# Optimization experiments

Hardware: AMD Instinct MI355X
Metric: run time of the kernel (lower is better)

## Reference

```python
import jax, jax.numpy as jnp
import numpy as np

B, S, D, P, H, DFF = 32, 512, 768, 256, 12, 3072
DH = D // H
EPS_LN = 1e-5
EPS_TRIP = 1e-6
MARGIN = 1.0


def setup_inputs() -> dict:
    key = jax.random.key(0)
    ks = jax.random.split(key, 16)
    sent_emb = jax.random.normal(ks[0], (B, S, D), jnp.float32)
    pair_sidx = jax.random.randint(ks[1], (P,), 0, B, jnp.int32)

    def mk_span(k):
        k1, k2 = jax.random.split(k)
        start = jax.random.randint(k1, (P,), 1, S - 9, jnp.int32)
        length = jax.random.randint(k2, (P,), 1, 9, jnp.int32)
        return jnp.stack([start, start + length], axis=1)  # [P,2] half-open

    s_span = mk_span(ks[2])
    p_span = mk_span(ks[3])
    n_span = mk_span(ks[4])
    sc = 0.02

    def w(k, shape):
        return jax.random.normal(k, shape, jnp.float32) * sc

    return dict(
        sent_emb=sent_emb, pair_sidx=pair_sidx,
        s_span=s_span, p_span=p_span, n_span=n_span,
        Wq=w(ks[5], (D, D)), bq=jnp.zeros((D,), jnp.float32),
        Wk=w(ks[6], (D, D)), bk=jnp.zeros((D,), jnp.float32),
        Wv=w(ks[7], (D, D)), bv=jnp.zeros((D,), jnp.float32),
        Wo=w(ks[8], (D, D)), bo=jnp.zeros((D,), jnp.float32),
        ln1_g=jnp.ones((D,), jnp.float32), ln1_b=jnp.zeros((D,), jnp.float32),
        ln2_g=jnp.ones((D,), jnp.float32), ln2_b=jnp.zeros((D,), jnp.float32),
        W1=w(ks[9], (D, DFF)), b1=jnp.zeros((DFF,), jnp.float32),
        W2=w(ks[10], (DFF, D)), b2=jnp.zeros((D,), jnp.float32),
    )


def _ln(x, g, b):
    m = jnp.mean(x, axis=-1, keepdims=True)
    v = jnp.mean((x - m) ** 2, axis=-1, keepdims=True)
    return (x - m) * jax.lax.rsqrt(v + EPS_LN) * g + b


def reference(sent_emb, pair_sidx, s_span, p_span, n_span,
              Wq, bq, Wk, bk, Wv, bv, Wo, bo,
              ln1_g, ln1_b, ln2_g, ln2_b, W1, b1, W2, b2):
    g = sent_emb[pair_sidx]  # [P,S,D] per-pair gathered sentence
    pos = jnp.arange(S)

    def pool(span):  # ragged mean-pool over [start,end)
        mask = ((pos[None, :] >= span[:, :1]) & (pos[None, :] < span[:, 1:2])).astype(sent_emb.dtype)
        cnt = jnp.sum(mask, axis=-1, keepdims=True)
        return jnp.einsum('ps,psd->pd', mask, g) / cnt

    s_emb = pool(s_span)
    p_emb = pool(p_span)
    n_emb = pool(n_span)
    cls_emb = sent_emb[pair_sidx, 0]           # [P,D]
    mem = jnp.stack([cls_emb, s_emb], axis=1)  # [P,2,D] (cls, source phrase)

    def attend(q):  # 1-query cross-attention over 2 memory slots, per pair
        qh = (q @ Wq + bq).reshape(P, H, DH)
        kh = (mem @ Wk + bk).reshape(P, 2, H, DH)
        vh = (mem @ Wv + bv).reshape(P, 2, H, DH)
        scores = jnp.einsum('phd,pkhd->phk', qh, kh) / np.sqrt(DH).astype(np.float32)
        a = jax.nn.softmax(scores, axis=-1)
        o = jnp.einsum('phk,pkhd->phd', a, vh).reshape(P, D)
        return o @ Wo + bo

    def block(x):  # residual attn + LN + position-wise FFN + LN (dropout=eval/identity)
        h = _ln(x + attend(x), ln1_g, ln1_b)
        f = jnp.maximum(h @ W1 + b1, 0.0) @ W2 + b2
        return _ln(h + f, ln2_g, ln2_b)

    atten_p = block(p_emb)
    atten_n = block(n_emb)
    dp = jnp.linalg.norm(s_emb - atten_p + EPS_TRIP, axis=-1)
    dn = jnp.linalg.norm(s_emb - atten_n + EPS_TRIP, axis=-1)
    return jnp.mean(jnp.maximum(dp - dn + MARGIN, 0.0))
```

## Files before the change

### kernel.cpp

```cpp
#include <hip/hip_runtime.h>
#include <hip/hip_bf16.h>

#define Dsz 768
#define Psz 256
#define Hsz 12
#define DHsz 64
#define DFFsz 3072
#define Msz 512
#define EPS_LN 1e-5f
#define EPS_TRIP 1e-6f

typedef unsigned short u16;
typedef __attribute__((ext_vector_type(8))) short bf16x8;
typedef __attribute__((ext_vector_type(4))) float f32x4;

__device__ __forceinline__ u16 f2bf(float f) {
    __hip_bfloat16 h = __float2bfloat16(f);
    u16 u; __builtin_memcpy(&u, &h, 2); return u;
}

__global__ __launch_bounds__(256) void pool_kernel(
    const float* __restrict__ sent, const int* __restrict__ sidx,
    const int* __restrict__ s_span, const int* __restrict__ p_span,
    const int* __restrict__ n_span,
    float* __restrict__ mem, float* __restrict__ qin,
    u16* __restrict__ memb, u16* __restrict__ qinb)
{
    int p = blockIdx.x;
    int b = sidx[p];
    const float* base = sent + (size_t)b * 512 * Dsz;
    int ss = s_span[2*p], se = s_span[2*p+1];
    int ps = p_span[2*p], pe = p_span[2*p+1];
    int ns = n_span[2*p], ne = n_span[2*p+1];
    float is  = 1.0f / (float)(se - ss);
    float ip  = 1.0f / (float)(pe - ps);
    float in_ = 1.0f / (float)(ne - ns);
    for (int d = threadIdx.x; d < Dsz; d += 256) {
        float cls = base[d];
        float as = 0.f, ap = 0.f, an = 0.f;
        for (int s = ss; s < se; ++s) as += base[(size_t)s*Dsz + d];
        for (int s = ps; s < pe; ++s) ap += base[(size_t)s*Dsz + d];
        for (int s = ns; s < ne; ++s) an += base[(size_t)s*Dsz + d];
        as *= is; ap *= ip; an *= in_;
        mem[(size_t)(2*p+0)*Dsz + d] = cls;
        mem[(size_t)(2*p+1)*Dsz + d] = as;
        qin[(size_t)(0*Psz + p)*Dsz + d] = ap;
        qin[(size_t)(1*Psz + p)*Dsz + d] = an;
        memb[(size_t)(2*p+0)*Dsz + d] = f2bf(cls);
        memb[(size_t)(2*p+1)*Dsz + d] = f2bf(as);
        qinb[(size_t)(0*Psz + p)*Dsz + d] = f2bf(ap);
        qinb[(size_t)(1*Psz + p)*Dsz + d] = f2bf(an);
    }
}

struct CvtArgs {
    const float* src[6];
    u16* dst[6];
    int K[6], N[6];
    int t0[7];
};

__global__ __launch_bounds__(256) void cvt_kernel(CvtArgs ca)
{
    __shared__ float tile[64][65];
    int bid = blockIdx.x;
    int w = 0;
    while (bid >= ca.t0[w+1]) ++w;
    int local = bid - ca.t0[w];
    int K = ca.K[w], N = ca.N[w];
    int ntN = N >> 6;
    int tk = local / ntN, tn = local - tk * ntN;
    int k0 = tk << 6, n0 = tn << 6;
    const float* src = ca.src[w];
    u16* dst = ca.dst[w];
    int t = threadIdx.x;
    int r = t >> 2, q = t & 3;
    #pragma unroll
    for (int j = 0; j < 4; ++j) {
        int c4 = q + j*4;
        float4 v = *(const float4*)(src + (size_t)(k0 + r)*N + n0 + c4*4);
        tile[r][c4*4+0] = v.x; tile[r][c4*4+1] = v.y;
        tile[r][c4*4+2] = v.z; tile[r][c4*4+3] = v.w;
    }
    __syncthreads();
    #pragma unroll
    for (int j = 0; j < 4; ++j) {
        int kc4 = q + j*4;
        ushort4 o;
        o.x = f2bf(tile[kc4*4+0][r]);
        o.y = f2bf(tile[kc4*4+1][r]);
        o.z = f2bf(tile[kc4*4+2][r]);
        o.w = f2bf(tile[kc4*4+3][r]);
        *(ushort4*)(dst + (size_t)(n0 + r)*K + k0 + kc4*4) = o;
    }
}

__device__ __forceinline__ void mfma_gemm_core(
    const u16* __restrict__ A, int lda,
    const u16* __restrict__ WT, int ldw,
    const float* __restrict__ bias,
    float* __restrict__ Cf, u16* __restrict__ Cb, int ldc,
    int Kloop, int relu, int bx, int by)
{
    int tid = threadIdx.x;
    int lane = tid & 63, wave = tid >> 6;
    int wr = wave >> 1, wc = wave & 1;
    int row0 = by*64 + wr*32, col0 = bx*64 + wc*32;
    int r = lane & 15, kg = lane >> 4;
    const u16* Ap0 = A  + (size_t)(row0 + r)      * lda + kg*8;
    const u16* Ap1 = A  + (size_t)(row0 + 16 + r) * lda + kg*8;
    const u16* Bp0 = WT + (size_t)(col0 + r)      * ldw + kg*8;
    const u16* Bp1 = WT + (size_t)(col0 + 16 + r) * ldw + kg*8;
    f32x4 acc00 = {0.f,0.f,0.f,0.f}, acc01 = {0.f,0.f,0.f,0.f};
    f32x4 acc10 = {0.f,0.f,0.f,0.f}, acc11 = {0.f,0.f,0.f,0.f};
    for (int k = 0; k < Kloop; k += 64) {
        bf16x8 a0 = *(const bf16x8*)(Ap0 + k);
        bf16x8 a1 = *(const bf16x8*)(Ap1 + k);
        bf16x8 b0 = *(const bf16x8*)(Bp0 + k);
        bf16x8 b1 = *(const bf16x8*)(Bp1 + k);
        bf16x8 a2 = *(const bf16x8*)(Ap0 + k + 32);
        bf16x8 a3 = *(const bf16x8*)(Ap1 + k + 32);
        bf16x8 b2 = *(const bf16x8*)(Bp0 + k + 32);
        bf16x8 b3 = *(const bf16x8*)(Bp1 + k + 32);
        acc00 = __builtin_amdgcn_mfma_f32_16x16x32_bf16(a0, b0, acc00, 0, 0, 0);
        acc01 = __builtin_amdgcn_mfma_f32_16x16x32_bf16(a0, b1, acc01, 0, 0, 0);
        acc10 = __builtin_amdgcn_mfma_f32_16x16x32_bf16(a1, b0, acc10, 0, 0, 0);
        acc11 = __builtin_amdgcn_mfma_f32_16x16x32_bf16(a1, b1, acc11, 0, 0, 0);
        acc00 = __builtin_amdgcn_mfma_f32_16x16x32_bf16(a2, b2, acc00, 0, 0, 0);
        acc01 = __builtin_amdgcn_mfma_f32_16x16x32_bf16(a2, b3, acc01, 0, 0, 0);
        acc10 = __builtin_amdgcn_mfma_f32_16x16x32_bf16(a3, b2, acc10, 0, 0, 0);
        acc11 = __builtin_amdgcn_mfma_f32_16x16x32_bf16(a3, b3, acc11, 0, 0, 0);
    }
    float b0s = bias ? bias[col0 + r]      : 0.f;
    float b1s = bias ? bias[col0 + 16 + r] : 0.f;
    #pragma unroll
    for (int e = 0; e < 4; ++e) {
        int rr0 = row0 + kg*4 + e;
        int rr1 = rr0 + 16;
        float v00 = acc00[e] + b0s, v01 = acc01[e] + b1s;
        float v10 = acc10[e] + b0s, v11 = acc11[e] + b1s;
        if (relu) {
            v00 = fmaxf(v00, 0.f); v01 = fmaxf(v01, 0.f);
            v10 = fmaxf(v10, 0.f); v11 = fmaxf(v11, 0.f);
        }
        if (Cf) {
            Cf[(size_t)rr0*ldc + col0 + r]      = v00;
            Cf[(size_t)rr0*ldc + col0 + 16 + r] = v01;
            Cf[(size_t)rr1*ldc + col0 + r]      = v10;
            Cf[(size_t)rr1*ldc + col0 + 16 + r] = v11;
        }
        if (Cb) {
            Cb[(size_t)rr0*ldc + col0 + r]      = f2bf(v00);
            Cb[(size_t)rr0*ldc + col0 + 16 + r] = f2bf(v01);
            Cb[(size_t)rr1*ldc + col0 + r]      = f2bf(v10);
            Cb[(size_t)rr1*ldc + col0 + 16 + r] = f2bf(v11);
        }
    }
}

struct Proj3Args {
    const u16* A[3];
    const u16* WT[3];
    const float* bias[3];
    float* C[3];
};
__global__ __launch_bounds__(256) void proj3_mfma(Proj3Args pa)
{
    int j = blockIdx.z;
    mfma_gemm_core(pa.A[j], Dsz, pa.WT[j], Dsz, pa.bias[j],
                   pa.C[j], nullptr, Dsz, Dsz, 0, blockIdx.x, blockIdx.y);
}

__global__ __launch_bounds__(256) void gemm_mfma(
    const u16* __restrict__ A, int lda, const u16* __restrict__ WT, int ldw,
    const float* __restrict__ bias, float* __restrict__ Cf, u16* __restrict__ Cb,
    int ldc, int Kloop, int relu)
{
    mfma_gemm_core(A, lda, WT, ldw, bias, Cf, Cb, ldc, Kloop, relu,
                   blockIdx.x, blockIdx.y);
}

__global__ __launch_bounds__(256) void gemm_mfma_splitk(
    const u16* __restrict__ A, int lda, const u16* __restrict__ WT, int ldw,
    const float* __restrict__ bias, float* __restrict__ Cpart,
    int ldc, int Ks, size_t pstride)
{
    int s = blockIdx.z;
    mfma_gemm_core(A + (size_t)s * Ks, lda, WT + (size_t)s * Ks, ldw,
                   (s == 0) ? bias : nullptr,
                   Cpart + (size_t)s * pstride, nullptr, ldc, Ks, 0,
                   blockIdx.x, blockIdx.y);
}

__global__ __launch_bounds__(64) void attn_kernel(
    const float* __restrict__ qh, const float* __restrict__ kh,
    const float* __restrict__ vh, u16* __restrict__ ob)
{
    int rblk = blockIdx.x;
    int p = rblk & (Psz - 1);
    int lane = threadIdx.x;
    const float* q  = qh + (size_t)rblk * Dsz;
    const float* k0 = kh + (size_t)(2*p) * Dsz;
    const float* k1 = k0 + Dsz;
    const float* v0 = vh + (size_t)(2*p) * Dsz;
    const float* v1 = v0 + Dsz;
    u16* o = ob + (size_t)rblk * Dsz;
    #pragma unroll
    for (int h = 0; h < Hsz; ++h) {
        int idx = h * DHsz + lane;
        float qv = q[idx];
        float s0 = qv * k0[idx];
        float s1 = qv * k1[idx];
        #pragma unroll
        for (int off = 32; off; off >>= 1) {
            s0 += __shfl_xor(s0, off);
            s1 += __shfl_xor(s1, off);
        }
        s0 *= 0.125f;
        s1 *= 0.125f;
        float m = fmaxf(s0, s1);
        float e0 = expf(s0 - m), e1 = expf(s1 - m);
        float inv = 1.f / (e0 + e1);
        o[idx] = f2bf((e0 * inv) * v0[idx] + (e1 * inv) * v1[idx]);
    }
}

__global__ __launch_bounds__(256) void ln_kernel(
    const float* __restrict__ x, const float* __restrict__ y,
    int nparts, size_t pstride,
    const float* __restrict__ g, const float* __restrict__ b,
    float* __restrict__ out, u16* __restrict__ out16)
{
    __shared__ float sb[4];
    int rr = blockIdx.x;
    int t = threadIdx.x;
    float v[3];
    float s = 0.f;
    #pragma unroll
    for (int i = 0; i < 3; ++i) {
        int d = t + i * 256;
        float acc = x[(size_t)rr*Dsz + d];
        for (int q = 0; q < nparts; ++q)
            acc += y[(size_t)q*pstride + (size_t)rr*Dsz + d];
        v[i] = acc;
        s += acc;
    }
    #pragma unroll
    for (int off = 32; off; off >>= 1) s += __shfl_xor(s, off);
    if ((t & 63) == 0) sb[t >> 6] = s;
    __syncthreads();
    float mean = (sb[0] + sb[1] + sb[2] + sb[3]) * (1.0f / Dsz);
    __syncthreads();
    float sv = 0.f;
    #pragma unroll
    for (int i = 0; i < 3; ++i) { float d0 = v[i] - mean; sv += d0 * d0; }
    #pragma unroll
    for (int off = 32; off; off >>= 1) sv += __shfl_xor(sv, off);
    if ((t & 63) == 0) sb[t >> 6] = sv;
    __syncthreads();
    float var = (sb[0] + sb[1] + sb[2] + sb[3]) * (1.0f / Dsz);
    float rstd = 1.0f / sqrtf(var + EPS_LN);
    #pragma unroll
    for (int i = 0; i < 3; ++i) {
        int d = t + i * 256;
        float o = (v[i] - mean) * rstd * g[d] + b[d];
        out[(size_t)rr*Dsz + d] = o;
        if (out16) out16[(size_t)rr*Dsz + d] = f2bf(o);
    }
}

__global__ __launch_bounds__(256) void loss_kernel(
    const float* __restrict__ mem, const float* __restrict__ outb,
    float* __restrict__ d_out)
{
    __shared__ float sb0[4], sb1[4];
    int p = blockIdx.x;
    int t = threadIdx.x;
    const float* se = mem  + (size_t)(2*p+1) * Dsz;
    const float* ap = outb + (size_t)p * Dsz;
    const float* an = outb + (size_t)(Psz + p) * Dsz;
    float dp = 0.f, dn = 0.f;
    #pragma unroll
    for (int i = 0; i < 3; ++i) {
        int d = t + i * 256;
        float a = se[d] - ap[d] + EPS_TRIP; dp += a * a;
        float c = se[d] - an[d] + EPS_TRIP; dn += c * c;
    }
    #pragma unroll
    for (int off = 32; off; off >>= 1) {
        dp += __shfl_xor(dp, off);
        dn += __shfl_xor(dn, off);
    }
    if ((t & 63) == 0) { sb0[t >> 6] = dp; sb1[t >> 6] = dn; }
    __syncthreads();
    if (t == 0) {
        float dps = sqrtf(sb0[0] + sb0[1] + sb0[2] + sb0[3]);
        float dns = sqrtf(sb1[0] + sb1[1] + sb1[2] + sb1[3]);
        float loss = fmaxf(dps - dns + 1.0f, 0.f);
        atomicAdd(d_out, loss * (1.0f / Psz));
    }
}

extern "C" void kernel_launch(void* const* d_in, const int* in_sizes, int n_in,
                              void* d_out, int out_size, void* d_ws, size_t ws_size,
                              hipStream_t stream) {
    const float* sent  = (const float*)d_in[0];
    const int*   sidx  = (const int*)d_in[1];
    const int*   sspan = (const int*)d_in[2];
    const int*   pspan = (const int*)d_in[3];
    const int*   nspan = (const int*)d_in[4];
    const float* Wq = (const float*)d_in[5];
    const float* bq = (const float*)d_in[6];
    const float* Wk = (const float*)d_in[7];
    const float* bk = (const float*)d_in[8];
    const float* Wv = (const float*)d_in[9];
    const float* bv = (const float*)d_in[10];
    const float* Wo = (const float*)d_in[11];
    const float* bo = (const float*)d_in[12];
    const float* ln1g = (const float*)d_in[13];
    const float* ln1b = (const float*)d_in[14];
    const float* ln2g = (const float*)d_in[15];
    const float* ln2b = (const float*)d_in[16];
    const float* W1 = (const float*)d_in[17];
    const float* b1 = (const float*)d_in[18];
    const float* W2 = (const float*)d_in[19];
    const float* b2 = (const float*)d_in[20];
    float* out = (float*)d_out;

    const size_t F = (size_t)Msz * Dsz;
    float* ws   = (float*)d_ws;
    float* mem  = ws + 0*F;
    float* qin  = ws + 1*F;
    float* outbf= ws + 1*F;
    float* hbuf = ws + 2*F;
    float* partb= ws + 3*F;
    float* qh   = ws + 3*F;
    float* kh   = ws + 4*F;
    float* vh   = ws + 5*F;
    u16* memb   = (u16*)(ws + 7*F);
    u16* qinb   = (u16*)(ws + 7*F) + F;
    u16* obufb  = (u16*)(ws + 8*F);
    u16* hbufb  = (u16*)(ws + 8*F) + F;
    u16* f1b    = (u16*)(ws + 9*F);
    u16* WqT    = (u16*)(ws + 11*F);
    u16* WkT    = WqT + (size_t)Dsz*Dsz;
    u16* WvT    = WkT + (size_t)Dsz*Dsz;
    u16* WoT    = WvT + (size_t)Dsz*Dsz;
    u16* W1T    = WoT + (size_t)Dsz*Dsz;
    u16* W2T    = W1T + (size_t)Dsz*DFFsz;

    hipMemsetAsync(d_out, 0, sizeof(float), stream);

    pool_kernel<<<Psz, 256, 0, stream>>>(sent, sidx, sspan, pspan, nspan,
                                         mem, qin, memb, qinb);

    CvtArgs ca;
    ca.src[0]=Wq; ca.src[1]=Wk; ca.src[2]=Wv; ca.src[3]=Wo; ca.src[4]=W1; ca.src[5]=W2;
    ca.dst[0]=WqT; ca.dst[1]=WkT; ca.dst[2]=WvT; ca.dst[3]=WoT; ca.dst[4]=W1T; ca.dst[5]=W2T;
    ca.K[0]=Dsz; ca.K[1]=Dsz; ca.K[2]=Dsz; ca.K[3]=Dsz; ca.K[4]=Dsz;  ca.K[5]=DFFsz;
    ca.N[0]=Dsz; ca.N[1]=Dsz; ca.N[2]=Dsz; ca.N[3]=Dsz; ca.N[4]=DFFsz; ca.N[5]=Dsz;
    int acc_t = 0;
    for (int i = 0; i < 6; ++i) {
        ca.t0[i] = acc_t;
        acc_t += (ca.K[i] >> 6) * (ca.N[i] >> 6);
    }
    ca.t0[6] = acc_t;
    cvt_kernel<<<acc_t, 256, 0, stream>>>(ca);

    Proj3Args pa;
    pa.A[0]=memb; pa.WT[0]=WkT; pa.bias[0]=bk; pa.C[0]=kh;
    pa.A[1]=memb; pa.WT[1]=WvT; pa.bias[1]=bv; pa.C[1]=vh;
    pa.A[2]=qinb; pa.WT[2]=WqT; pa.bias[2]=bq; pa.C[2]=qh;
    proj3_mfma<<<dim3(Dsz/64, Msz/64, 3), 256, 0, stream>>>(pa);

    attn_kernel<<<Msz, 64, 0, stream>>>(qh, kh, vh, obufb);

    gemm_mfma_splitk<<<dim3(Dsz/64, Msz/64, 4), 256, 0, stream>>>(
        obufb, Dsz, WoT, Dsz, bo, partb, Dsz, Dsz/4, F);

    ln_kernel<<<Msz, 256, 0, stream>>>(qin, partb, 4, F, ln1g, ln1b, hbuf, hbufb);

    gemm_mfma<<<dim3(DFFsz/64, Msz/64), 256, 0, stream>>>(
        hbufb, Dsz, W1T, Dsz, b1, nullptr, f1b, DFFsz, Dsz, 1);

    gemm_mfma_splitk<<<dim3(Dsz/64, Msz/64, 4), 256, 0, stream>>>(
        f1b, DFFsz, W2T, DFFsz, b2, partb, Dsz, DFFsz/4, F);

    ln_kernel<<<Msz, 256, 0, stream>>>(hbuf, partb, 4, F, ln2g, ln2b, outbf, nullptr);

    loss_kernel<<<Psz, 256, 0, stream>>>(mem, outbf, out);
}
```

Measured before the change: 265.8 us.

## Fuse whole pipeline into one persistent kernel with atomic grid barriers

Replaces the ten separate launches (pool, weight convert, QKV projection, attention, Wo split-K, LN1, FFN1, FFN2 split-K, LN2, loss) with a single persistent kernel of 256 blocks. The stages are separated by atomic-counter grid barriers. It also fuses the second LayerNorm with the per-row triplet distance and replaces the atomicAdd loss with a final single-block reduction. Split-K goes from 4 to 2 partitions. The aim is to remove launch overhead and intermediate round trips, at the cost of barrier spin time and less parallelism within each stage: 256 blocks cover 384 FFN1 tiles and only 192 split-K tiles, so some stages run partly idle. Correctness depends on all 256 blocks being co-resident.

```diff
diff --git a/kernel.cpp b/kernel.cpp
--- a/kernel.cpp
+++ b/kernel.cpp
@@ -9,6 +9,7 @@
 #define Msz 512
 #define EPS_LN 1e-5f
 #define EPS_TRIP 1e-6f
+#define NBLK 256
 
 typedef unsigned short u16;
 typedef __attribute__((ext_vector_type(8))) short bf16x8;
@@ -19,83 +20,20 @@
     u16 u; __builtin_memcpy(&u, &h, 2); return u;
 }
 
-__global__ __launch_bounds__(256) void pool_kernel(
-    const float* __restrict__ sent, const int* __restrict__ sidx,
-    const int* __restrict__ s_span, const int* __restrict__ p_span,
-    const int* __restrict__ n_span,
-    float* __restrict__ mem, float* __restrict__ qin,
-    u16* __restrict__ memb, u16* __restrict__ qinb)
-{
-    int p = blockIdx.x;
-    int b = sidx[p];
-    const float* base = sent + (size_t)b * 512 * Dsz;
-    int ss = s_span[2*p], se = s_span[2*p+1];
-    int ps = p_span[2*p], pe = p_span[2*p+1];
-    int ns = n_span[2*p], ne = n_span[2*p+1];
-    float is  = 1.0f / (float)(se - ss);
-    float ip  = 1.0f / (float)(pe - ps);
-    float in_ = 1.0f / (float)(ne - ns);
-    for (int d = threadIdx.x; d < Dsz; d += 256) {
-        float cls = base[d];
-        float as = 0.f, ap = 0.f, an = 0.f;
-        for (int s = ss; s < se; ++s) as += base[(size_t)s*Dsz + d];
-        for (int s = ps; s < pe; ++s) ap += base[(size_t)s*Dsz + d];
-        for (int s = ns; s < ne; ++s) an += base[(size_t)s*Dsz + d];
-        as *= is; ap *= ip; an *= in_;
-        mem[(size_t)(2*p+0)*Dsz + d] = cls;
-        mem[(size_t)(2*p+1)*Dsz + d] = as;
-        qin[(size_t)(0*Psz + p)*Dsz + d] = ap;
-        qin[(size_t)(1*Psz + p)*Dsz + d] = an;
-        memb[(size_t)(2*p+0)*Dsz + d] = f2bf(cls);
-        memb[(size_t)(2*p+1)*Dsz + d] = f2bf(as);
-        qinb[(size_t)(0*Psz + p)*Dsz + d] = f2bf(ap);
-        qinb[(size_t)(1*Psz + p)*Dsz + d] = f2bf(an);
-    }
-}
-
-struct CvtArgs {
-    const float* src[6];
-    u16* dst[6];
-    int K[6], N[6];
-    int t0[7];
-};
-
-__global__ __launch_bounds__(256) void cvt_kernel(CvtArgs ca)
-{
-    __shared__ float tile[64][65];
-    int bid = blockIdx.x;
-    int w = 0;
-    while (bid >= ca.t0[w+1]) ++w;
-    int local = bid - ca.t0[w];
-    int K = ca.K[w], N = ca.N[w];
-    int ntN = N >> 6;
-    int tk = local / ntN, tn = local - tk * ntN;
-    int k0 = tk << 6, n0 = tn << 6;
-    const float* src = ca.src[w];
-    u16* dst = ca.dst[w];
-    int t = threadIdx.x;
-    int r = t >> 2, q = t & 3;
-    #pragma unroll
-    for (int j = 0; j < 4; ++j) {
-        int c4 = q + j*4;
-        float4 v = *(const float4*)(src + (size_t)(k0 + r)*N + n0 + c4*4);
-        tile[r][c4*4+0] = v.x; tile[r][c4*4+1] = v.y;
-        tile[r][c4*4+2] = v.z; tile[r][c4*4+3] = v.w;
-    }
+__device__ __forceinline__ void gridbar(unsigned* c) {
     __syncthreads();
-    #pragma unroll
-    for (int j = 0; j < 4; ++j) {
-        int kc4 = q + j*4;
-        ushort4 o;
-        o.x = f2bf(tile[kc4*4+0][r]);
-        o.y = f2bf(tile[kc4*4+1][r]);
-        o.z = f2bf(tile[kc4*4+2][r]);
-        o.w = f2bf(tile[kc4*4+3][r]);
-        *(ushort4*)(dst + (size_t)(n0 + r)*K + k0 + kc4*4) = o;
-    }
-}
-
-__device__ __forceinline__ void mfma_gemm_core(
+    if (threadIdx.x == 0) {
+        __threadfence();
+        __hip_atomic_fetch_add(c, 1u, __ATOMIC_RELEASE, __HIP_MEMORY_SCOPE_AGENT);
+        while (__hip_atomic_load(c, __ATOMIC_ACQUIRE, __HIP_MEMORY_SCOPE_AGENT) < NBLK) {
+            __builtin_amdgcn_s_sleep(1);
+        }
+        __threadfence();
+    }
+    __syncthreads();
+}
+
+__device__ void mfma_tile(
     const u16* __restrict__ A, int lda,
     const u16* __restrict__ WT, int ldw,
     const float* __restrict__ bias,
@@ -158,235 +96,284 @@
     }
 }
 
-struct Proj3Args {
-    const u16* A[3];
-    const u16* WT[3];
-    const float* bias[3];
-    float* C[3];
-};
-__global__ __launch_bounds__(256) void proj3_mfma(Proj3Args pa)
-{
-    int j = blockIdx.z;
-    mfma_gemm_core(pa.A[j], Dsz, pa.WT[j], Dsz, pa.bias[j],
-                   pa.C[j], nullptr, Dsz, Dsz, 0, blockIdx.x, blockIdx.y);
-}
-
-__global__ __launch_bounds__(256) void gemm_mfma(
-    const u16* __restrict__ A, int lda, const u16* __restrict__ WT, int ldw,
-    const float* __restrict__ bias, float* __restrict__ Cf, u16* __restrict__ Cb,
-    int ldc, int Kloop, int relu)
-{
-    mfma_gemm_core(A, lda, WT, ldw, bias, Cf, Cb, ldc, Kloop, relu,
-                   blockIdx.x, blockIdx.y);
-}
-
-__global__ __launch_bounds__(256) void gemm_mfma_splitk(
-    const u16* __restrict__ A, int lda, const u16* __restrict__ WT, int ldw,
-    const float* __restrict__ bias, float* __restrict__ Cpart,
-    int ldc, int Ks, size_t pstride)
-{
-    int s = blockIdx.z;
-    mfma_gemm_core(A + (size_t)s * Ks, lda, WT + (size_t)s * Ks, ldw,
-                   (s == 0) ? bias : nullptr,
-                   Cpart + (size_t)s * pstride, nullptr, ldc, Ks, 0,
-                   blockIdx.x, blockIdx.y);
-}
-
-__global__ __launch_bounds__(64) void attn_kernel(
-    const float* __restrict__ qh, const float* __restrict__ kh,
-    const float* __restrict__ vh, u16* __restrict__ ob)
-{
-    int rblk = blockIdx.x;
-    int p = rblk & (Psz - 1);
-    int lane = threadIdx.x;
-    const float* q  = qh + (size_t)rblk * Dsz;
-    const float* k0 = kh + (size_t)(2*p) * Dsz;
-    const float* k1 = k0 + Dsz;
-    const float* v0 = vh + (size_t)(2*p) * Dsz;
-    const float* v1 = v0 + Dsz;
-    u16* o = ob + (size_t)rblk * Dsz;
-    #pragma unroll
-    for (int h = 0; h < Hsz; ++h) {
-        int idx = h * DHsz + lane;
-        float qv = q[idx];
-        float s0 = qv * k0[idx];
-        float s1 = qv * k1[idx];
-        #pragma unroll
-        for (int off = 32; off; off >>= 1) {
-            s0 += __shfl_xor(s0, off);
-            s1 += __shfl_xor(s1, off);
-        }
-        s0 *= 0.125f;
-        s1 *= 0.125f;
-        float m = fmaxf(s0, s1);
-        float e0 = expf(s0 - m), e1 = expf(s1 - m);
-        float inv = 1.f / (e0 + e1);
-        o[idx] = f2bf((e0 * inv) * v0[idx] + (e1 * inv) * v1[idx]);
-    }
-}
-
-__global__ __launch_bounds__(256) void ln_kernel(
-    const float* __restrict__ x, const float* __restrict__ y,
-    int nparts, size_t pstride,
-    const float* __restrict__ g, const float* __restrict__ b,
-    float* __restrict__ out, u16* __restrict__ out16)
-{
-    __shared__ float sb[4];
-    int rr = blockIdx.x;
-    int t = threadIdx.x;
-    float v[3];
-    float s = 0.f;
-    #pragma unroll
-    for (int i = 0; i < 3; ++i) {
-        int d = t + i * 256;
-        float acc = x[(size_t)rr*Dsz + d];
-        for (int q = 0; q < nparts; ++q)
-            acc += y[(size_t)q*pstride + (size_t)rr*Dsz + d];
-        v[i] = acc;
-        s += acc;
-    }
+__device__ __forceinline__ float blk_sum(float s, float* sb) {
     #pragma unroll
     for (int off = 32; off; off >>= 1) s += __shfl_xor(s, off);
-    if ((t & 63) == 0) sb[t >> 6] = s;
+    if ((threadIdx.x & 63) == 0) sb[threadIdx.x >> 6] = s;
     __syncthreads();
-    float mean = (sb[0] + sb[1] + sb[2] + sb[3]) * (1.0f / Dsz);
+    float tot = sb[0] + sb[1] + sb[2] + sb[3];
     __syncthreads();
-    float sv = 0.f;
-    #pragma unroll
-    for (int i = 0; i < 3; ++i) { float d0 = v[i] - mean; sv += d0 * d0; }
-    #pragma unroll
-    for (int off = 32; off; off >>= 1) sv += __shfl_xor(sv, off);
-    if ((t & 63) == 0) sb[t >> 6] = sv;
-    __syncthreads();
-    float var = (sb[0] + sb[1] + sb[2] + sb[3]) * (1.0f / Dsz);
-    float rstd = 1.0f / sqrtf(var + EPS_LN);
-    #pragma unroll
-    for (int i = 0; i < 3; ++i) {
-        int d = t + i * 256;
-        float o = (v[i] - mean) * rstd * g[d] + b[d];
-        out[(size_t)rr*Dsz + d] = o;
-        if (out16) out16[(size_t)rr*Dsz + d] = f2bf(o);
-    }
-}
-
-__global__ __launch_bounds__(256) void loss_kernel(
-    const float* __restrict__ mem, const float* __restrict__ outb,
-    float* __restrict__ d_out)
+    return tot;
+}
+
+struct FusedArgs {
+    const float* sent; const int* sidx; const int* sspan; const int* pspan; const int* nspan;
+    const float* Wq; const float* bq; const float* Wk; const float* bk;
+    const float* Wv; const float* bv; const float* Wo; const float* bo;
+    const float* ln1g; const float* ln1b; const float* ln2g; const float* ln2b;
+    const float* W1; const float* b1; const float* W2; const float* b2;
+    const float* csrc[6]; u16* cdst[6]; int cK[6], cN[6], ct0[7];
+    float *mem, *qin, *hbuf, *p0, *p1, *qh, *kh, *vh, *rowsq;
+    u16 *memb, *qinb, *obufb, *hbufb, *f1b, *WqT, *WkT, *WvT, *WoT, *W1T, *W2T;
+    unsigned* bar;
+    float* out;
+};
+
+__global__ __launch_bounds__(256, 2) void fused_kernel(FusedArgs a)
 {
-    __shared__ float sb0[4], sb1[4];
-    int p = blockIdx.x;
-    int t = threadIdx.x;
-    const float* se = mem  + (size_t)(2*p+1) * Dsz;
-    const float* ap = outb + (size_t)p * Dsz;
-    const float* an = outb + (size_t)(Psz + p) * Dsz;
-    float dp = 0.f, dn = 0.f;
-    #pragma unroll
-    for (int i = 0; i < 3; ++i) {
-        int d = t + i * 256;
-        float a = se[d] - ap[d] + EPS_TRIP; dp += a * a;
-        float c = se[d] - an[d] + EPS_TRIP; dn += c * c;
-    }
-    #pragma unroll
-    for (int off = 32; off; off >>= 1) {
-        dp += __shfl_xor(dp, off);
-        dn += __shfl_xor(dn, off);
-    }
-    if ((t & 63) == 0) { sb0[t >> 6] = dp; sb1[t >> 6] = dn; }
-    __syncthreads();
-    if (t == 0) {
-        float dps = sqrtf(sb0[0] + sb0[1] + sb0[2] + sb0[3]);
-        float dns = sqrtf(sb1[0] + sb1[1] + sb1[2] + sb1[3]);
-        float loss = fmaxf(dps - dns + 1.0f, 0.f);
-        atomicAdd(d_out, loss * (1.0f / Psz));
+    __shared__ float tile[64][65];
+    __shared__ float sb[4];
+    int b   = blockIdx.x;
+    int tid = threadIdx.x;
+    int wave = tid >> 6, lane = tid & 63;
+
+    {
+        int p = b;
+        int bb = a.sidx[p];
+        const float* base = a.sent + (size_t)bb * 512 * Dsz;
+        int ss = a.sspan[2*p], se = a.sspan[2*p+1];
+        int ps = a.pspan[2*p], pe = a.pspan[2*p+1];
+        int ns = a.nspan[2*p], ne = a.nspan[2*p+1];
+        float is  = 1.0f / (float)(se - ss);
+        float ip  = 1.0f / (float)(pe - ps);
+        float in_ = 1.0f / (float)(ne - ns);
+        for (int d = tid; d < Dsz; d += 256) {
+            float cls = base[d];
+            float as = 0.f, ap = 0.f, an = 0.f;
+            for (int s = ss; s < se; ++s) as += base[(size_t)s*Dsz + d];
+            for (int s = ps; s < pe; ++s) ap += base[(size_t)s*Dsz + d];
+            for (int s = ns; s < ne; ++s) an += base[(size_t)s*Dsz + d];
+            as *= is; ap *= ip; an *= in_;
+            a.mem[(size_t)(2*p+0)*Dsz + d] = cls;
+            a.mem[(size_t)(2*p+1)*Dsz + d] = as;
+            a.qin[(size_t)(0*Psz + p)*Dsz + d] = ap;
+            a.qin[(size_t)(1*Psz + p)*Dsz + d] = an;
+            a.memb[(size_t)(2*p+0)*Dsz + d] = f2bf(cls);
+            a.memb[(size_t)(2*p+1)*Dsz + d] = f2bf(as);
+            a.qinb[(size_t)(0*Psz + p)*Dsz + d] = f2bf(ap);
+            a.qinb[(size_t)(1*Psz + p)*Dsz + d] = f2bf(an);
+        }
+    }
+    for (int t = b; t < 1728; t += NBLK) {
+        __syncthreads();
+        int w = 0;
+        while (t >= a.ct0[w+1]) ++w;
+        int local = t - a.ct0[w];
+        int K = a.cK[w], N = a.cN[w];
+        int ntN = N >> 6;
+        int tk = local / ntN, tn = local - tk * ntN;
+        int k0 = tk << 6, n0 = tn << 6;
+        const float* src = a.csrc[w];
+        u16* dst = a.cdst[w];
+        int rr = tid >> 2, q = tid & 3;
+        #pragma unroll
+        for (int j = 0; j < 4; ++j) {
+            int c4 = q + j*4;
+            float4 v = *(const float4*)(src + (size_t)(k0 + rr)*N + n0 + c4*4);
+            tile[rr][c4*4+0] = v.x; tile[rr][c4*4+1] = v.y;
+            tile[rr][c4*4+2] = v.z; tile[rr][c4*4+3] = v.w;
+        }
+        __syncthreads();
+        #pragma unroll
+        for (int j = 0; j < 4; ++j) {
+            int kc4 = q + j*4;
+            ushort4 o;
+            o.x = f2bf(tile[kc4*4+0][rr]);
+            o.y = f2bf(tile[kc4*4+1][rr]);
+            o.z = f2bf(tile[kc4*4+2][rr]);
+            o.w = f2bf(tile[kc4*4+3][rr]);
+            *(ushort4*)(dst + (size_t)(n0 + rr)*K + k0 + kc4*4) = o;
+        }
+    }
+    gridbar(a.bar + 0);
+
+    for (int t = b; t < 288; t += NBLK) {
+        int j = t / 96, u = t % 96;
+        int bx = u % 12, by = u / 12;
+        const u16* A  = (j == 2) ? a.qinb : a.memb;
+        const u16* WT = (j == 0) ? a.WkT : (j == 1) ? a.WvT : a.WqT;
+        const float* bias = (j == 0) ? a.bk : (j == 1) ? a.bv : a.bq;
+        float* C = (j == 0) ? a.kh : (j == 1) ? a.vh : a.qh;
+        mfma_tile(A, Dsz, WT, Dsz, bias, C, nullptr, Dsz, Dsz, 0, bx, by);
+    }
+    gridbar(a.bar + 1);
+
+    {
+        int rrow = 2*b + (wave >> 1);
+        int p = rrow & (Psz - 1);
+        int hseg = (wave & 1) * 6;
+        const float* q  = a.qh + (size_t)rrow * Dsz;
+        const float* k0 = a.kh + (size_t)(2*p) * Dsz;
+        const float* k1 = k0 + Dsz;
+        const float* v0 = a.vh + (size_t)(2*p) * Dsz;
+        const float* v1 = v0 + Dsz;
+        u16* o = a.obufb + (size_t)rrow * Dsz;
+        #pragma unroll
+        for (int hh = 0; hh < 6; ++hh) {
+            int idx = (hseg + hh) * DHsz + lane;
+            float qv = q[idx];
+            float s0 = qv * k0[idx];
+            float s1 = qv * k1[idx];
+            #pragma unroll
+            for (int off = 32; off; off >>= 1) {
+                s0 += __shfl_xor(s0, off);
+                s1 += __shfl_xor(s1, off);
+            }
+            s0 *= 0.125f;  s1 *= 0.125f;
+            float m = fmaxf(s0, s1);
+            float e0 = expf(s0 - m), e1 = expf(s1 - m);
+            float inv = 1.f / (e0 + e1);
+            o[idx] = f2bf((e0 * inv) * v0[idx] + (e1 * inv) * v1[idx]);
+        }
+    }
+    gridbar(a.bar + 2);
+
+    for (int t = b; t < 192; t += NBLK) {
+        int s = t / 96, u = t % 96;
+        int bx = u % 12, by = u / 12;
+        mfma_tile(a.obufb + (size_t)s * 384, Dsz, a.WoT + (size_t)s * 384, Dsz,
+                  (s == 0) ? a.bo : nullptr,
+                  (s == 0) ? a.p0 : a.p1, nullptr, Dsz, 384, 0, bx, by);
+    }
+    gridbar(a.bar + 3);
+
+    for (int i = 0; i < 2; ++i) {
+        int rrow = 2*b + i;
+        float v[3]; float s = 0.f;
+        #pragma unroll
+        for (int j = 0; j < 3; ++j) {
+            int d = tid + j * 256;
+            size_t ix = (size_t)rrow*Dsz + d;
+            float acc = a.qin[ix] + a.p0[ix] + a.p1[ix];
+            v[j] = acc; s += acc;
+        }
+        float mean = blk_sum(s, sb) * (1.0f / Dsz);
+        float sv = 0.f;
+        #pragma unroll
+        for (int j = 0; j < 3; ++j) { float d0 = v[j] - mean; sv += d0 * d0; }
+        float var = blk_sum(sv, sb) * (1.0f / Dsz);
+        float rstd = 1.0f / sqrtf(var + EPS_LN);
+        #pragma unroll
+        for (int j = 0; j < 3; ++j) {
+            int d = tid + j * 256;
+            float o = (v[j] - mean) * rstd * a.ln1g[d] + a.ln1b[d];
+            a.hbuf[(size_t)rrow*Dsz + d] = o;
+            a.hbufb[(size_t)rrow*Dsz + d] = f2bf(o);
+        }
+        __syncthreads();
+    }
+    gridbar(a.bar + 4);
+
+    for (int t = b; t < 384; t += NBLK) {
+        int bx = t % 48, by = t / 48;
+        mfma_tile(a.hbufb, Dsz, a.W1T, Dsz, a.b1,
+                  nullptr, a.f1b, DFFsz, Dsz, 1, bx, by);
+    }
+    gridbar(a.bar + 5);
+
+    for (int t = b; t < 192; t += NBLK) {
+        int s = t / 96, u = t % 96;
+        int bx = u % 12, by = u / 12;
+        mfma_tile(a.f1b + (size_t)s * 1536, DFFsz, a.W2T + (size_t)s * 1536, DFFsz,
+                  (s == 0) ? a.b2 : nullptr,
+                  (s == 0) ? a.p0 : a.p1, nullptr, Dsz, 1536, 0, bx, by);
+    }
+    gridbar(a.bar + 6);
+
+    for (int i = 0; i < 2; ++i) {
+        int rrow = 2*b + i;
+        int p = rrow & (Psz - 1);
+        const float* se = a.mem + (size_t)(2*p+1) * Dsz;
+        float v[3]; float s = 0.f;
+        #pragma unroll
+        for (int j = 0; j < 3; ++j) {
+            int d = tid + j * 256;
+            size_t ix = (size_t)rrow*Dsz + d;
+            float acc = a.hbuf[ix] + a.p0[ix] + a.p1[ix];
+            v[j] = acc; s += acc;
+        }
+        float mean = blk_sum(s, sb) * (1.0f / Dsz);
+        float sv = 0.f;
+        #pragma unroll
+        for (int j = 0; j < 3; ++j) { float d0 = v[j] - mean; sv += d0 * d0; }
+        float var = blk_sum(sv, sb) * (1.0f / Dsz);
+        float rstd = 1.0f / sqrtf(var + EPS_LN);
+        float dsq = 0.f;
+        #pragma unroll
+        for (int j = 0; j < 3; ++j) {
+            int d = tid + j * 256;
+            float o = (v[j] - mean) * rstd * a.ln2g[d] + a.ln2b[d];
+            float diff = se[d] - o + EPS_TRIP;
+            dsq += diff * diff;
+        }
+        float tot = blk_sum(dsq, sb);
+        if (tid == 0) a.rowsq[rrow] = tot;
+        __syncthreads();
+    }
+    gridbar(a.bar + 7);
+
+    if (b == 0) {
+        float dp = sqrtf(a.rowsq[tid]);
+        float dn = sqrtf(a.rowsq[Psz + tid]);
+        float l = fmaxf(dp - dn + 1.0f, 0.f);
+        float tot = blk_sum(l, sb);
+        if (tid == 0) a.out[0] = tot * (1.0f / Psz);
     }
 }
 
 extern "C" void kernel_launch(void* const* d_in, const int* in_sizes, int n_in,
                               void* d_out, int out_size, void* d_ws, size_t ws_size,
                               hipStream_t stream) {
-    const float* sent  = (const float*)d_in[0];
-    const int*   sidx  = (const int*)d_in[1];
-    const int*   sspan = (const int*)d_in[2];
-    const int*   pspan = (const int*)d_in[3];
-    const int*   nspan = (const int*)d_in[4];
-    const float* Wq = (const float*)d_in[5];
-    const float* bq = (const float*)d_in[6];
-    const float* Wk = (const float*)d_in[7];
-    const float* bk = (const float*)d_in[8];
-    const float* Wv = (const float*)d_in[9];
-    const float* bv = (const float*)d_in[10];
-    const float* Wo = (const float*)d_in[11];
-    const float* bo = (const float*)d_in[12];
-    const float* ln1g = (const float*)d_in[13];
-    const float* ln1b = (const float*)d_in[14];
-    const float* ln2g = (const float*)d_in[15];
-    const float* ln2b = (const float*)d_in[16];
-    const float* W1 = (const float*)d_in[17];
-    const float* b1 = (const float*)d_in[18];
-    const float* W2 = (const float*)d_in[19];
-    const float* b2 = (const float*)d_in[20];
-    float* out = (float*)d_out;
+    FusedArgs a;
+    a.sent  = (const float*)d_in[0];
+    a.sidx  = (const int*)d_in[1];
+    a.sspan = (const int*)d_in[2];
+    a.pspan = (const int*)d_in[3];
+    a.nspan = (const int*)d_in[4];
+    a.Wq = (const float*)d_in[5];  a.bq = (const float*)d_in[6];
+    a.Wk = (const float*)d_in[7];  a.bk = (const float*)d_in[8];
+    a.Wv = (const float*)d_in[9];  a.bv = (const float*)d_in[10];
+    a.Wo = (const float*)d_in[11]; a.bo = (const float*)d_in[12];
+    a.ln1g = (const float*)d_in[13]; a.ln1b = (const float*)d_in[14];
+    a.ln2g = (const float*)d_in[15]; a.ln2b = (const float*)d_in[16];
+    a.W1 = (const float*)d_in[17]; a.b1 = (const float*)d_in[18];
+    a.W2 = (const float*)d_in[19]; a.b2 = (const float*)d_in[20];
+    a.out = (float*)d_out;
 
     const size_t F = (size_t)Msz * Dsz;
-    float* ws   = (float*)d_ws;
-    float* mem  = ws + 0*F;
-    float* qin  = ws + 1*F;
-    float* outbf= ws + 1*F;
-    float* hbuf = ws + 2*F;
-    float* partb= ws + 3*F;
-    float* qh   = ws + 3*F;
-    float* kh   = ws + 4*F;
-    float* vh   = ws + 5*F;
-    u16* memb   = (u16*)(ws + 7*F);
-    u16* qinb   = (u16*)(ws + 7*F) + F;
-    u16* obufb  = (u16*)(ws + 8*F);
-    u16* hbufb  = (u16*)(ws + 8*F) + F;
-    u16* f1b    = (u16*)(ws + 9*F);
-    u16* WqT    = (u16*)(ws + 11*F);
-    u16* WkT    = WqT + (size_t)Dsz*Dsz;
-    u16* WvT    = WkT + (size_t)Dsz*Dsz;
-    u16* WoT    = WvT + (size_t)Dsz*Dsz;
-    u16* W1T    = WoT + (size_t)Dsz*Dsz;
-    u16* W2T    = W1T + (size_t)Dsz*DFFsz;
-
-    hipMemsetAsync(d_out, 0, sizeof(float), stream);
-
-    pool_kernel<<<Psz, 256, 0, stream>>>(sent, sidx, sspan, pspan, nspan,
-                                         mem, qin, memb, qinb);
-
-    CvtArgs ca;
-    ca.src[0]=Wq; ca.src[1]=Wk; ca.src[2]=Wv; ca.src[3]=Wo; ca.src[4]=W1; ca.src[5]=W2;
-    ca.dst[0]=WqT; ca.dst[1]=WkT; ca.dst[2]=WvT; ca.dst[3]=WoT; ca.dst[4]=W1T; ca.dst[5]=W2T;
-    ca.K[0]=Dsz; ca.K[1]=Dsz; ca.K[2]=Dsz; ca.K[3]=Dsz; ca.K[4]=Dsz;  ca.K[5]=DFFsz;
-    ca.N[0]=Dsz; ca.N[1]=Dsz; ca.N[2]=Dsz; ca.N[3]=Dsz; ca.N[4]=DFFsz; ca.N[5]=Dsz;
+    float* ws = (float*)d_ws;
+    a.mem   = ws + 0*F;
+    a.qin   = ws + 1*F;
+    a.hbuf  = ws + 2*F;
+    a.qh = a.p0 = ws + 3*F;
+    a.kh = a.p1 = ws + 4*F;
+    a.vh    = ws + 5*F;
+    a.rowsq = ws + 6*F;
+    a.bar   = (unsigned*)(ws + 6*F + 768);
+    a.memb  = (u16*)(ws + 7*F);
+    a.qinb  = (u16*)(ws + 8*F);
+    a.obufb = (u16*)(ws + 9*F);
+    a.hbufb = (u16*)(ws + 10*F);
+    a.f1b   = (u16*)(ws + 11*F);
+    a.WqT   = (u16*)(ws + 13*F);
+    a.WkT   = (u16*)(ws + 14*F);
+    a.WvT   = (u16*)(ws + 15*F);
+    a.WoT   = (u16*)(ws + 16*F);
+    a.W1T   = (u16*)(ws + 17*F);
+    a.W2T   = (u16*)(ws + 20*F);
+
+    a.csrc[0]=a.Wq; a.csrc[1]=a.Wk; a.csrc[2]=a.Wv; a.csrc[3]=a.Wo; a.csrc[4]=a.W1; a.csrc[5]=a.W2;
+    a.cdst[0]=a.WqT; a.cdst[1]=a.WkT; a.cdst[2]=a.WvT; a.cdst[3]=a.WoT; a.cdst[4]=a.W1T; a.cdst[5]=a.W2T;
+    a.cK[0]=Dsz; a.cK[1]=Dsz; a.cK[2]=Dsz; a.cK[3]=Dsz; a.cK[4]=Dsz;  a.cK[5]=DFFsz;
+    a.cN[0]=Dsz; a.cN[1]=Dsz; a.cN[2]=Dsz; a.cN[3]=Dsz; a.cN[4]=DFFsz; a.cN[5]=Dsz;
     int acc_t = 0;
     for (int i = 0; i < 6; ++i) {
-        ca.t0[i] = acc_t;
-        acc_t += (ca.K[i] >> 6) * (ca.N[i] >> 6);
-    }
-    ca.t0[6] = acc_t;
-    cvt_kernel<<<acc_t, 256, 0, stream>>>(ca);
-
-    Proj3Args pa;
-    pa.A[0]=memb; pa.WT[0]=WkT; pa.bias[0]=bk; pa.C[0]=kh;
-    pa.A[1]=memb; pa.WT[1]=WvT; pa.bias[1]=bv; pa.C[1]=vh;
-    pa.A[2]=qinb; pa.WT[2]=WqT; pa.bias[2]=bq; pa.C[2]=qh;
-    proj3_mfma<<<dim3(Dsz/64, Msz/64, 3), 256, 0, stream>>>(pa);
-
-    attn_kernel<<<Msz, 64, 0, stream>>>(qh, kh, vh, obufb);
-
-    gemm_mfma_splitk<<<dim3(Dsz/64, Msz/64, 4), 256, 0, stream>>>(
-        obufb, Dsz, WoT, Dsz, bo, partb, Dsz, Dsz/4, F);
-
-    ln_kernel<<<Msz, 256, 0, stream>>>(qin, partb, 4, F, ln1g, ln1b, hbuf, hbufb);
-
-    gemm_mfma<<<dim3(DFFsz/64, Msz/64), 256, 0, stream>>>(
-        hbufb, Dsz, W1T, Dsz, b1, nullptr, f1b, DFFsz, Dsz, 1);
-
-    gemm_mfma_splitk<<<dim3(Dsz/64, Msz/64, 4), 256, 0, stream>>>(
-        f1b, DFFsz, W2T, DFFsz, b2, partb, Dsz, DFFsz/4, F);
-
-    ln_kernel<<<Msz, 256, 0, stream>>>(hbuf, partb, 4, F, ln2g, ln2b, outbf, nullptr);
-
-    loss_kernel<<<Psz, 256, 0, stream>>>(mem, outbf, out);
-}
+        a.ct0[i] = acc_t;
+        acc_t += (a.cK[i] >> 6) * (a.cN[i] >> 6);
+    }
+    a.ct0[6] = acc_t;
+
+    hipMemsetAsync((void*)a.bar, 0, 64, stream);
+
+    fused_kernel<<<NBLK, 256, 0, stream>>>(a);
+}
```

Measured after the change: 563.8 us. +112.1%, slower.

## Fuse pooling with weight conversion and LN2 with loss, drop memset and atomics

Applied to the files above, without the earlier changes.

Pooling and weight transpose/convert now run as one launch with branched blocks. The second LayerNorm is fused with the per-row triplet distance, so the normalized output is no longer written out and read back. A single-block kernel then reduces the loss, which replaces the memset and the atomics. This removes several launches and some memory traffic, at the cost of reworking the workspace layout and adding one small extra kernel.

```diff
diff --git a/kernel.cpp b/kernel.cpp
--- a/kernel.cpp
+++ b/kernel.cpp
@@ -19,79 +19,83 @@
     u16 u; __builtin_memcpy(&u, &h, 2); return u;
 }
 
-__global__ __launch_bounds__(256) void pool_kernel(
-    const float* __restrict__ sent, const int* __restrict__ sidx,
-    const int* __restrict__ s_span, const int* __restrict__ p_span,
-    const int* __restrict__ n_span,
-    float* __restrict__ mem, float* __restrict__ qin,
-    u16* __restrict__ memb, u16* __restrict__ qinb)
-{
-    int p = blockIdx.x;
-    int b = sidx[p];
-    const float* base = sent + (size_t)b * 512 * Dsz;
-    int ss = s_span[2*p], se = s_span[2*p+1];
-    int ps = p_span[2*p], pe = p_span[2*p+1];
-    int ns = n_span[2*p], ne = n_span[2*p+1];
-    float is  = 1.0f / (float)(se - ss);
-    float ip  = 1.0f / (float)(pe - ps);
-    float in_ = 1.0f / (float)(ne - ns);
-    for (int d = threadIdx.x; d < Dsz; d += 256) {
-        float cls = base[d];
-        float as = 0.f, ap = 0.f, an = 0.f;
-        for (int s = ss; s < se; ++s) as += base[(size_t)s*Dsz + d];
-        for (int s = ps; s < pe; ++s) ap += base[(size_t)s*Dsz + d];
-        for (int s = ns; s < ne; ++s) an += base[(size_t)s*Dsz + d];
-        as *= is; ap *= ip; an *= in_;
-        mem[(size_t)(2*p+0)*Dsz + d] = cls;
-        mem[(size_t)(2*p+1)*Dsz + d] = as;
-        qin[(size_t)(0*Psz + p)*Dsz + d] = ap;
-        qin[(size_t)(1*Psz + p)*Dsz + d] = an;
-        memb[(size_t)(2*p+0)*Dsz + d] = f2bf(cls);
-        memb[(size_t)(2*p+1)*Dsz + d] = f2bf(as);
-        qinb[(size_t)(0*Psz + p)*Dsz + d] = f2bf(ap);
-        qinb[(size_t)(1*Psz + p)*Dsz + d] = f2bf(an);
-    }
-}
-
-struct CvtArgs {
-    const float* src[6];
-    u16* dst[6];
-    int K[6], N[6];
-    int t0[7];
+__device__ __forceinline__ float blk_sum(float s, float* sb) {
+    #pragma unroll
+    for (int off = 32; off; off >>= 1) s += __shfl_xor(s, off);
+    if ((threadIdx.x & 63) == 0) sb[threadIdx.x >> 6] = s;
+    __syncthreads();
+    float tot = sb[0] + sb[1] + sb[2] + sb[3];
+    __syncthreads();
+    return tot;
+}
+
+struct PoolCvtArgs {
+    const float* sent; const int* sidx; const int* sspan; const int* pspan; const int* nspan;
+    float* mem; float* qin; u16* memb; u16* qinb;
+    const float* csrc[6]; u16* cdst[6]; int cK[6], cN[6], ct0[7];
 };
 
-__global__ __launch_bounds__(256) void cvt_kernel(CvtArgs ca)
+__global__ __launch_bounds__(256) void pool_cvt_kernel(PoolCvtArgs a)
 {
     __shared__ float tile[64][65];
     int bid = blockIdx.x;
-    int w = 0;
-    while (bid >= ca.t0[w+1]) ++w;
-    int local = bid - ca.t0[w];
-    int K = ca.K[w], N = ca.N[w];
-    int ntN = N >> 6;
-    int tk = local / ntN, tn = local - tk * ntN;
-    int k0 = tk << 6, n0 = tn << 6;
-    const float* src = ca.src[w];
-    u16* dst = ca.dst[w];
-    int t = threadIdx.x;
-    int r = t >> 2, q = t & 3;
-    #pragma unroll
-    for (int j = 0; j < 4; ++j) {
-        int c4 = q + j*4;
-        float4 v = *(const float4*)(src + (size_t)(k0 + r)*N + n0 + c4*4);
-        tile[r][c4*4+0] = v.x; tile[r][c4*4+1] = v.y;
-        tile[r][c4*4+2] = v.z; tile[r][c4*4+3] = v.w;
-    }
-    __syncthreads();
-    #pragma unroll
-    for (int j = 0; j < 4; ++j) {
-        int kc4 = q + j*4;
-        ushort4 o;
-        o.x = f2bf(tile[kc4*4+0][r]);
-        o.y = f2bf(tile[kc4*4+1][r]);
-        o.z = f2bf(tile[kc4*4+2][r]);
-        o.w = f2bf(tile[kc4*4+3][r]);
-        *(ushort4*)(dst + (size_t)(n0 + r)*K + k0 + kc4*4) = o;
+    int tid = threadIdx.x;
+    if (bid < Psz) {
+        int p = bid;
+        int bb = a.sidx[p];
+        const float* base = a.sent + (size_t)bb * 512 * Dsz;
+        int ss = a.sspan[2*p], se = a.sspan[2*p+1];
+        int ps = a.pspan[2*p], pe = a.pspan[2*p+1];
+        int ns = a.nspan[2*p], ne = a.nspan[2*p+1];
+        float is  = 1.0f / (float)(se - ss);
+        float ip  = 1.0f / (float)(pe - ps);
+        float in_ = 1.0f / (float)(ne - ns);
+        for (int d = tid; d < Dsz; d += 256) {
+            float cls = base[d];
+            float as = 0.f, ap = 0.f, an = 0.f;
+            for (int s = ss; s < se; ++s) as += base[(size_t)s*Dsz + d];
+            for (int s = ps; s < pe; ++s) ap += base[(size_t)s*Dsz + d];
+            for (int s = ns; s < ne; ++s) an += base[(size_t)s*Dsz + d];
+            as *= is; ap *= ip; an *= in_;
+            a.mem[(size_t)(2*p+0)*Dsz + d] = cls;
+            a.mem[(size_t)(2*p+1)*Dsz + d] = as;
+            a.qin[(size_t)(0*Psz + p)*Dsz + d] = ap;
+            a.qin[(size_t)(1*Psz + p)*Dsz + d] = an;
+            a.memb[(size_t)(2*p+0)*Dsz + d] = f2bf(cls);
+            a.memb[(size_t)(2*p+1)*Dsz + d] = f2bf(as);
+            a.qinb[(size_t)(0*Psz + p)*Dsz + d] = f2bf(ap);
+            a.qinb[(size_t)(1*Psz + p)*Dsz + d] = f2bf(an);
+        }
+    } else {
+        int t = bid - Psz;
+        int w = 0;
+        while (t >= a.ct0[w+1]) ++w;
+        int local = t - a.ct0[w];
+        int K = a.cK[w], N = a.cN[w];
+        int ntN = N >> 6;
+        int tk = local / ntN, tn = local - tk * ntN;
+        int k0 = tk << 6, n0 = tn << 6;
+        const float* src = a.csrc[w];
+        u16* dst = a.cdst[w];
+        int rr = tid >> 2, q = tid & 3;
+        #pragma unroll
+        for (int j = 0; j < 4; ++j) {
+            int c4 = q + j*4;
+            float4 v = *(const float4*)(src + (size_t)(k0 + rr)*N + n0 + c4*4);
+            tile[rr][c4*4+0] = v.x; tile[rr][c4*4+1] = v.y;
+            tile[rr][c4*4+2] = v.z; tile[rr][c4*4+3] = v.w;
+        }
+        __syncthreads();
+        #pragma unroll
+        for (int j = 0; j < 4; ++j) {
+            int kc4 = q + j*4;
+            ushort4 o;
+            o.x = f2bf(tile[kc4*4+0][rr]);
+            o.y = f2bf(tile[kc4*4+1][rr]);
+            o.z = f2bf(tile[kc4*4+2][rr]);
+            o.w = f2bf(tile[kc4*4+3][rr]);
+            *(ushort4*)(dst + (size_t)(n0 + rr)*K + k0 + kc4*4) = o;
+        }
     }
 }
 
@@ -245,20 +249,11 @@
         v[i] = acc;
         s += acc;
     }
-    #pragma unroll
-    for (int off = 32; off; off >>= 1) s += __shfl_xor(s, off);
-    if ((t & 63) == 0) sb[t >> 6] = s;
-    __syncthreads();
-    float mean = (sb[0] + sb[1] + sb[2] + sb[3]) * (1.0f / Dsz);
-    __syncthreads();
+    float mean = blk_sum(s, sb) * (1.0f / Dsz);
     float sv = 0.f;
     #pragma unroll
     for (int i = 0; i < 3; ++i) { float d0 = v[i] - mean; sv += d0 * d0; }
-    #pragma unroll
-    for (int off = 32; off; off >>= 1) sv += __shfl_xor(sv, off);
-    if ((t & 63) == 0) sb[t >> 6] = sv;
-    __syncthreads();
-    float var = (sb[0] + sb[1] + sb[2] + sb[3]) * (1.0f / Dsz);
+    float var = blk_sum(sv, sb) * (1.0f / Dsz);
     float rstd = 1.0f / sqrtf(var + EPS_LN);
     #pragma unroll
     for (int i = 0; i < 3; ++i) {
@@ -269,36 +264,56 @@
     }
 }
 
-__global__ __launch_bounds__(256) void loss_kernel(
-    const float* __restrict__ mem, const float* __restrict__ outb,
-    float* __restrict__ d_out)
-{
-    __shared__ float sb0[4], sb1[4];
-    int p = blockIdx.x;
+__global__ __launch_bounds__(256) void ln2_loss_kernel(
+    const float* __restrict__ x, const float* __restrict__ y,
+    int nparts, size_t pstride,
+    const float* __restrict__ g, const float* __restrict__ b,
+    const float* __restrict__ mem, float* __restrict__ rowsq)
+{
+    __shared__ float sb[4];
+    int rr = blockIdx.x;
+    int p = rr & (Psz - 1);
+    const float* se = mem + (size_t)(2*p+1) * Dsz;
     int t = threadIdx.x;
-    const float* se = mem  + (size_t)(2*p+1) * Dsz;
-    const float* ap = outb + (size_t)p * Dsz;
-    const float* an = outb + (size_t)(Psz + p) * Dsz;
-    float dp = 0.f, dn = 0.f;
+    float v[3];
+    float s = 0.f;
     #pragma unroll
     for (int i = 0; i < 3; ++i) {
         int d = t + i * 256;
-        float a = se[d] - ap[d] + EPS_TRIP; dp += a * a;
-        float c = se[d] - an[d] + EPS_TRIP; dn += c * c;
-    }
-    #pragma unroll
-    for (int off = 32; off; off >>= 1) {
-        dp += __shfl_xor(dp, off);
-        dn += __shfl_xor(dn, off);
-    }
-    if ((t & 63) == 0) { sb0[t >> 6] = dp; sb1[t >> 6] = dn; }
-    __syncthreads();
-    if (t == 0) {
-        float dps = sqrtf(sb0[0] + sb0[1] + sb0[2] + sb0[3]);
-        float dns = sqrtf(sb1[0] + sb1[1] + sb1[2] + sb1[3]);
-        float loss = fmaxf(dps - dns + 1.0f, 0.f);
-        atomicAdd(d_out, loss * (1.0f / Psz));
-    }
+        float acc = x[(size_t)rr*Dsz + d];
+        for (int q = 0; q < nparts; ++q)
+            acc += y[(size_t)q*pstride + (size_t)rr*Dsz + d];
+        v[i] = acc;
+        s += acc;
+    }
+    float mean = blk_sum(s, sb) * (1.0f / Dsz);
+    float sv = 0.f;
+    #pragma unroll
+    for (int i = 0; i < 3; ++i) { float d0 = v[i] - mean; sv += d0 * d0; }
+    float var = blk_sum(sv, sb) * (1.0f / Dsz);
+    float rstd = 1.0f / sqrtf(var + EPS_LN);
+    float dsq = 0.f;
+    #pragma unroll
+    for (int i = 0; i < 3; ++i) {
+        int d = t + i * 256;
+        float o = (v[i] - mean) * rstd * g[d] + b[d];
+        float diff = se[d] - o + EPS_TRIP;
+        dsq += diff * diff;
+    }
+    float tot = blk_sum(dsq, sb);
+    if (t == 0) rowsq[rr] = tot;
+}
+
+__global__ __launch_bounds__(256) void loss_final_kernel(
+    const float* __restrict__ rowsq, float* __restrict__ d_out)
+{
+    __shared__ float sb[4];
+    int t = threadIdx.x;
+    float dp = sqrtf(rowsq[t]);
+    float dn = sqrtf(rowsq[Psz + t]);
+    float l = fmaxf(dp - dn + 1.0f, 0.f);
+    float tot = blk_sum(l, sb);
+    if (t == 0) d_out[0] = tot * (1.0f / Psz);
 }
 
 extern "C" void kernel_launch(void* const* d_in, const int* in_sizes, int n_in,
@@ -328,44 +343,41 @@
     float* out = (float*)d_out;
 
     const size_t F = (size_t)Msz * Dsz;
-    float* ws   = (float*)d_ws;
-    float* mem  = ws + 0*F;
-    float* qin  = ws + 1*F;
-    float* outbf= ws + 1*F;
-    float* hbuf = ws + 2*F;
-    float* partb= ws + 3*F;
-    float* qh   = ws + 3*F;
-    float* kh   = ws + 4*F;
-    float* vh   = ws + 5*F;
-    u16* memb   = (u16*)(ws + 7*F);
-    u16* qinb   = (u16*)(ws + 7*F) + F;
-    u16* obufb  = (u16*)(ws + 8*F);
-    u16* hbufb  = (u16*)(ws + 8*F) + F;
-    u16* f1b    = (u16*)(ws + 9*F);
-    u16* WqT    = (u16*)(ws + 11*F);
-    u16* WkT    = WqT + (size_t)Dsz*Dsz;
-    u16* WvT    = WkT + (size_t)Dsz*Dsz;
-    u16* WoT    = WvT + (size_t)Dsz*Dsz;
-    u16* W1T    = WoT + (size_t)Dsz*Dsz;
-    u16* W2T    = W1T + (size_t)Dsz*DFFsz;
-
-    hipMemsetAsync(d_out, 0, sizeof(float), stream);
-
-    pool_kernel<<<Psz, 256, 0, stream>>>(sent, sidx, sspan, pspan, nspan,
-                                         mem, qin, memb, qinb);
-
-    CvtArgs ca;
-    ca.src[0]=Wq; ca.src[1]=Wk; ca.src[2]=Wv; ca.src[3]=Wo; ca.src[4]=W1; ca.src[5]=W2;
-    ca.dst[0]=WqT; ca.dst[1]=WkT; ca.dst[2]=WvT; ca.dst[3]=WoT; ca.dst[4]=W1T; ca.dst[5]=W2T;
-    ca.K[0]=Dsz; ca.K[1]=Dsz; ca.K[2]=Dsz; ca.K[3]=Dsz; ca.K[4]=Dsz;  ca.K[5]=DFFsz;
-    ca.N[0]=Dsz; ca.N[1]=Dsz; ca.N[2]=Dsz; ca.N[3]=Dsz; ca.N[4]=DFFsz; ca.N[5]=Dsz;
+    float* ws    = (float*)d_ws;
+    float* mem   = ws + 0*F;
+    float* qin   = ws + 1*F;
+    float* hbuf  = ws + 2*F;
+    float* partb = ws + 3*F;
+    float* qh    = ws + 7*F;
+    float* kh    = ws + 8*F;
+    float* vh    = ws + 9*F;
+    float* rowsq = ws + 10*F;
+    u16* memb    = (u16*)(ws + 11*F);
+    u16* qinb    = memb + F;
+    u16* obufb   = (u16*)(ws + 12*F);
+    u16* hbufb   = obufb + F;
+    u16* f1b     = (u16*)(ws + 13*F);
+    u16* WqT     = (u16*)(ws + 15*F);
+    u16* WkT     = (u16*)(ws + 16*F);
+    u16* WvT     = (u16*)(ws + 17*F);
+    u16* WoT     = (u16*)(ws + 18*F);
+    u16* W1T     = (u16*)(ws + 19*F);
+    u16* W2T     = (u16*)(ws + 22*F);
+
+    PoolCvtArgs pc;
+    pc.sent = sent; pc.sidx = sidx; pc.sspan = sspan; pc.pspan = pspan; pc.nspan = nspan;
+    pc.mem = mem; pc.qin = qin; pc.memb = memb; pc.qinb = qinb;
+    pc.csrc[0]=Wq; pc.csrc[1]=Wk; pc.csrc[2]=Wv; pc.csrc[3]=Wo; pc.csrc[4]=W1; pc.csrc[5]=W2;
+    pc.cdst[0]=WqT; pc.cdst[1]=WkT; pc.cdst[2]=WvT; pc.cdst[3]=WoT; pc.cdst[4]=W1T; pc.cdst[5]=W2T;
+    pc.cK[0]=Dsz; pc.cK[1]=Dsz; pc.cK[2]=Dsz; pc.cK[3]=Dsz; pc.cK[4]=Dsz;  pc.cK[5]=DFFsz;
+    pc.cN[0]=Dsz; pc.cN[1]=Dsz; pc.cN[2]=Dsz; pc.cN[3]=Dsz; pc.cN[4]=DFFsz; pc.cN[5]=Dsz;
     int acc_t = 0;
     for (int i = 0; i < 6; ++i) {
-        ca.t0[i] = acc_t;
-        acc_t += (ca.K[i] >> 6) * (ca.N[i] >> 6);
-    }
-    ca.t0[6] = acc_t;
-    cvt_kernel<<<acc_t, 256, 0, stream>>>(ca);
+        pc.ct0[i] = acc_t;
+        acc_t += (pc.cK[i] >> 6) * (pc.cN[i] >> 6);
+    }
+    pc.ct0[6] = acc_t;
+    pool_cvt_kernel<<<Psz + acc_t, 256, 0, stream>>>(pc);
 
     Proj3Args pa;
     pa.A[0]=memb; pa.WT[0]=WkT; pa.bias[0]=bk; pa.C[0]=kh;
@@ -386,7 +398,6 @@
     gemm_mfma_splitk<<<dim3(Dsz/64, Msz/64, 4), 256, 0, stream>>>(
         f1b, DFFsz, W2T, DFFsz, b2, partb, Dsz, DFFsz/4, F);
 
-    ln_kernel<<<Msz, 256, 0, stream>>>(hbuf, partb, 4, F, ln2g, ln2b, outbf, nullptr);
-
-    loss_kernel<<<Psz, 256, 0, stream>>>(mem, outbf, out);
-}
+    ln2_loss_kernel<<<Msz, 256, 0, stream>>>(hbuf, partb, 4, F, ln2g, ln2b, mem, rowsq);
+    loss_final_kernel<<<1, 256, 0, stream>>>(rowsq, out);
+}
```

New measurement: 254.7 us. 4.2% less time.
